# Performance work log

Measured on AMD Instinct MI355X. Metric: run time of the kernel, lower is better.

The kernel has to match this reference:

```python
import jax, jax.numpy as jnp
import numpy as np

NUM_OUT_POINTS = 8192  # init kwarg num_out_points


def setup_inputs() -> dict:
    key = jax.random.key(0)
    B, C, N = 32, 64, 65536
    x = jax.random.normal(key, (B, C, N), dtype=jnp.float32)
    return {"x": x}


def reference(x):
    # x: [B, C, N]. For each batch element draw a random permutation of the
    # N points and keep the first NUM_OUT_POINTS indices, then gather.
    B, C, N = x.shape
    keys = jax.random.split(jax.random.key(1), B)
    # idx: [B, K] int32, each row a prefix of an independent permutation of N
    idx = jax.vmap(lambda k: jax.random.permutation(k, N)[:NUM_OUT_POINTS])(keys)
    idx = idx.astype(jnp.int32)
    # gather along point axis: y[b, c, k] = x[b, c, idx[b, k]]
    y = jnp.take_along_axis(x, idx[:, None, :].astype(jnp.int64), axis=2)
    return y
```

## Files before the change

### kernel.cpp

```cpp
#include <hip/hip_runtime.h>
#include <stdint.h>

#define B_SZ 32
#define C_SZ 64
#define N_SZ 65536
#define K_SZ 8192
#define BCAP 384
#define NHEAD 48
#define JCAP 80

__device__ __forceinline__ uint32_t rotl32(uint32_t v, int r) {
  return (v << r) | (v >> (32 - r));
}

__device__ __forceinline__ void threefry2x32(uint32_t k0, uint32_t k1,
                                             uint32_t x0, uint32_t x1,
                                             uint32_t& o0, uint32_t& o1) {
  const uint32_t ks2 = k0 ^ k1 ^ 0x1BD11BDAu;
  x0 += k0; x1 += k1;
#define TF_R(r) { x0 += x1; x1 = rotl32(x1, (r)); x1 ^= x0; }
  TF_R(13) TF_R(15) TF_R(26) TF_R(6)   x0 += k1;  x1 += ks2 + 1u;
  TF_R(17) TF_R(29) TF_R(16) TF_R(24)  x0 += ks2; x1 += k0  + 2u;
  TF_R(13) TF_R(15) TF_R(26) TF_R(6)   x0 += k0;  x1 += k1  + 3u;
  TF_R(17) TF_R(29) TF_R(16) TF_R(24)  x0 += k1;  x1 += ks2 + 4u;
  TF_R(13) TF_R(15) TF_R(26) TF_R(6)   x0 += ks2; x1 += k0  + 5u;
#undef TF_R
  o0 = x0; o1 = x1;
}

__device__ __forceinline__ void subkey_for_round(int b, int round,
                                                 uint32_t& sk0, uint32_t& sk1) {
  uint32_t c0, c1;
  threefry2x32(0u, 1u, 0u, (uint32_t)b, c0, c1);
  for (int r = 0; r < round; ++r) {
    uint32_t n0, n1;
    threefry2x32(c0, c1, 0u, 0u, n0, n1);
    c0 = n0; c1 = n1;
  }
  threefry2x32(c0, c1, 0u, 1u, sk0, sk1);
}

__device__ __forceinline__ uint32_t block_excl_scan(uint32_t h, int t,
                                                    uint32_t* __restrict__ wsum) {
  const int lane = t & 63, w = t >> 6;
  uint32_t inc = h;
#pragma unroll
  for (int off = 1; off < 64; off <<= 1) {
    const uint32_t y = __shfl_up(inc, off, 64);
    if (lane >= off) inc += y;
  }
  if (lane == 63) wsum[w] = inc;
  __syncthreads();
  uint32_t woff = 0;
#pragma unroll
  for (int w2 = 0; w2 < 4; ++w2)
    if (w2 < w) woff += wsum[w2];
  return woff + inc - h;
}

__global__ __launch_bounds__(256) void zero_cnt(uint32_t* __restrict__ z) {
  z[blockIdx.x * 256 + threadIdx.x] = 0;
}

__global__ __launch_bounds__(256) void gen_scatter1(uint64_t* __restrict__ BVfix,
                                                    uint32_t* __restrict__ cnt1) {
  __shared__ uint32_t lcnt[256];
  __shared__ uint32_t gb[256];
  const int t = threadIdx.x, chunk = blockIdx.x, b = blockIdx.y;
  lcnt[t] = 0; __syncthreads();
  uint32_t sk0, sk1;
  subkey_for_round(b, 0, sk0, sk1);
  uint64_t v[16]; uint32_t r[16], dg[16];
  const int base = chunk * 4096;
#pragma unroll
  for (int e = 0; e < 16; ++e) {
    const int i = base + e * 256 + t;
    uint32_t o0, o1;
    threefry2x32(sk0, sk1, 0u, (uint32_t)i, o0, o1);
    const uint32_t bits = o0 ^ o1;
    v[e] = ((uint64_t)bits << 16) | (uint64_t)i;
    dg[e] = bits >> 24;
    r[e] = atomicAdd(&lcnt[dg[e]], 1u);
  }
  __syncthreads();
  if (lcnt[t]) gb[t] = atomicAdd(&cnt1[b * 256 + t], lcnt[t]);
  __syncthreads();
#pragma unroll
  for (int e = 0; e < 16; ++e) {
    const uint32_t slot = gb[dg[e]] + r[e];
    if (slot < BCAP)
      BVfix[((size_t)(b * 256 + dg[e])) * BCAP + slot] = v[e];
  }
}

__global__ __launch_bounds__(256) void rank_sort1(const uint64_t* __restrict__ BVfix,
                                                  const uint32_t* __restrict__ cnt1,
                                                  uint16_t* __restrict__ S1v) {
  __shared__ uint32_t sub[BCAP];
  __shared__ uint16_t dg[BCAP];
  __shared__ uint16_t idxt[BCAP];
  __shared__ uint32_t hist[256];
  __shared__ uint32_t cur[256];
  __shared__ uint32_t base2[257];
  __shared__ uint32_t wsum[4];
  __shared__ uint32_t sh_bn[2];
  const int t = threadIdx.x, u = blockIdx.x, b = blockIdx.y;

  {
    uint32_t hh = cnt1[b * 256 + t];
    if (hh > BCAP) hh = BCAP;
    const uint32_t excl0 = block_excl_scan(hh, t, wsum);
    if (t == u) { sh_bn[0] = excl0; sh_bn[1] = hh; }
  }
  __syncthreads();
  const uint32_t base = sh_bn[0];
  const uint32_t n = sh_bn[1];
  const uint64_t* __restrict__ g = BVfix + ((size_t)(b * 256 + u)) * BCAP;

  hist[t] = 0; __syncthreads();
  uint64_t rec[2] = {0, 0};
#pragma unroll
  for (int w = 0; w < 2; ++w) {
    const int e = t + w * 256;
    if (e < (int)n) {
      rec[w] = g[e];
      const uint32_t key = (uint32_t)(rec[w] >> 16);
      const uint32_t d = (key >> 16) & 0xFFu;
      sub[e] = ((key & 0xFFFFu) << 16) | (uint32_t)(rec[w] & 0xFFFFull);
      dg[e] = (uint16_t)d;
      atomicAdd(&hist[d], 1u);
    }
  }
  __syncthreads();
  const uint32_t h = hist[t];
  const uint32_t excl = block_excl_scan(h, t, wsum);
  base2[t] = excl;
  cur[t] = excl;
  if (t == 255) base2[256] = excl + h;
  __syncthreads();
#pragma unroll
  for (int w = 0; w < 2; ++w) {
    const int e = t + w * 256;
    if (e < (int)n) idxt[atomicAdd(&cur[dg[e]], 1u)] = (uint16_t)e;
  }
  __syncthreads();
  uint16_t* __restrict__ out = S1v + (size_t)b * N_SZ + base;
#pragma unroll
  for (int w = 0; w < 2; ++w) {
    const int e = t + w * 256;
    if (e < (int)n) {
      const uint32_t d = dg[e], s = sub[e];
      const uint32_t lo = base2[d], hi = base2[d + 1];
      uint32_t r = 0;
      for (uint32_t i = lo; i < hi; ++i) r += (sub[idxt[i]] < s) ? 1u : 0u;
      out[lo + r] = (uint16_t)(rec[w] & 0xFFFFull);
    }
  }
}

__global__ __launch_bounds__(256) void gen_scatter2(const uint16_t* __restrict__ S1v,
                                                    uint64_t* __restrict__ CVfix,
                                                    uint32_t* __restrict__ cnt2) {
  __shared__ uint32_t lcnt[256];
  __shared__ uint32_t gb[256];
  const int t = threadIdx.x, chunk = blockIdx.x, b = blockIdx.y;
  lcnt[t] = 0; __syncthreads();
  uint32_t sk0, sk1;
  subkey_for_round(b, 1, sk0, sk1);
  const uint16_t* __restrict__ s1 = S1v + (size_t)b * N_SZ;
  uint64_t v[16]; uint32_t r[16], dg[16];
  const int base = chunk * 4096;
#pragma unroll
  for (int e = 0; e < 16; ++e) {
    const int i = base + e * 256 + t;
    uint32_t o0, o1;
    threefry2x32(sk0, sk1, 0u, (uint32_t)i, o0, o1);
    const uint32_t bits = o0 ^ o1;
    dg[e] = bits >> 24;
    if (dg[e] < NHEAD) {
      v[e] = ((uint64_t)bits << 32) | ((uint64_t)(uint32_t)i << 16) | (uint64_t)s1[i];
      r[e] = atomicAdd(&lcnt[dg[e]], 1u);
    }
  }
  __syncthreads();
  if (t < NHEAD && lcnt[t]) gb[t] = atomicAdd(&cnt2[b * 256 + t], lcnt[t]);
  __syncthreads();
#pragma unroll
  for (int e = 0; e < 16; ++e) {
    if (dg[e] < NHEAD) {
      const uint32_t slot = gb[dg[e]] + r[e];
      if (slot < BCAP)
        CVfix[((size_t)(b * NHEAD + dg[e])) * BCAP + slot] = v[e];
    }
  }
}

__global__ __launch_bounds__(256) void finalize_rank(const uint64_t* __restrict__ CVfix,
                                                     const uint32_t* __restrict__ cnt2,
                                                     uint32_t* __restrict__ jcnt,
                                                     uint32_t* __restrict__ jb) {
  __shared__ uint32_t sub[BCAP];
  __shared__ uint16_t dg[BCAP];
  __shared__ uint16_t idxt[BCAP];
  __shared__ uint32_t hist[256];
  __shared__ uint32_t cur[256];
  __shared__ uint32_t base2[257];
  __shared__ uint32_t wsum[4];
  __shared__ uint32_t sh_bn[2];
  const int t = threadIdx.x, u = blockIdx.x, b = blockIdx.y;

  {
    uint32_t hh = 0;
    if (t < NHEAD) { hh = cnt2[b * 256 + t]; if (hh > BCAP) hh = BCAP; }
    const uint32_t excl0 = block_excl_scan(hh, t, wsum);
    if (t == u) { sh_bn[0] = excl0; sh_bn[1] = hh; }
  }
  __syncthreads();
  const uint32_t base = sh_bn[0];
  if (base >= K_SZ) return;
  const uint32_t n = sh_bn[1];
  const uint64_t* __restrict__ g = CVfix + ((size_t)(b * NHEAD + u)) * BCAP;

  hist[t] = 0; __syncthreads();
  uint64_t rec[2] = {0, 0};
#pragma unroll
  for (int w = 0; w < 2; ++w) {
    const int e = t + w * 256;
    if (e < (int)n) {
      rec[w] = g[e];
      const uint32_t key = (uint32_t)(rec[w] >> 32);
      const uint32_t d = (key >> 16) & 0xFFu;
      sub[e] = ((key & 0xFFFFu) << 16) | (uint32_t)((rec[w] >> 16) & 0xFFFFull);
      dg[e] = (uint16_t)d;
      atomicAdd(&hist[d], 1u);
    }
  }
  __syncthreads();
  const uint32_t h = hist[t];
  const uint32_t excl = block_excl_scan(h, t, wsum);
  base2[t] = excl;
  cur[t] = excl;
  if (t == 255) base2[256] = excl + h;
  __syncthreads();
#pragma unroll
  for (int w = 0; w < 2; ++w) {
    const int e = t + w * 256;
    if (e < (int)n) idxt[atomicAdd(&cur[dg[e]], 1u)] = (uint16_t)e;
  }
  __syncthreads();
#pragma unroll
  for (int w = 0; w < 2; ++w) {
    const int e = t + w * 256;
    if (e < (int)n) {
      const uint32_t d = dg[e], s = sub[e];
      const uint32_t lo = base2[d], hi = base2[d + 1];
      uint32_t r = 0;
      for (uint32_t i = lo; i < hi; ++i) r += (sub[idxt[i]] < s) ? 1u : 0u;
      const uint32_t q = base + lo + r;
      if (q < K_SZ) {
        const uint32_t j = (uint32_t)(rec[w] & 0xFFFFull);
        const uint32_t slot = atomicAdd(&jcnt[b * 256 + (j >> 8)], 1u);
        if (slot < JCAP)
          jb[((size_t)b * 256 + (j >> 8)) * JCAP + slot] = (j << 16) | q;
      }
    }
  }
}

__global__ __launch_bounds__(256) void compact_pairs(const uint32_t* __restrict__ jcnt,
                                                     const uint32_t* __restrict__ jb,
                                                     uint32_t* __restrict__ sp) {
  __shared__ uint32_t bases[256];
  __shared__ uint8_t map8[K_SZ];
  __shared__ uint32_t wsum[4];
  const int b = blockIdx.x, t = threadIdx.x;
  uint32_t c = jcnt[b * 256 + t];
  if (c > JCAP) c = JCAP;
  const uint32_t excl = block_excl_scan(c, t, wsum);
  bases[t] = excl;
  for (uint32_t i = 0; i < c; ++i)
    if (excl + i < K_SZ) map8[excl + i] = (uint8_t)t;
  __syncthreads();
  const uint32_t* __restrict__ jbb = jb + (size_t)b * 256 * JCAP;
  uint32_t* __restrict__ dst = sp + (size_t)b * K_SZ;
#pragma unroll 8
  for (int k = t; k < K_SZ; k += 256) {
    const uint32_t d = map8[k];
    dst[k] = jbb[d * JCAP + (k - bases[d])];
  }
}

__global__ __launch_bounds__(256) void gather_staged(const float* __restrict__ x,
                                                     const uint32_t* __restrict__ sp,
                                                     float* __restrict__ y) {
  __shared__ float row[K_SZ];
  const int t = threadIdx.x, c = blockIdx.x, b = blockIdx.y;
  const uint32_t* __restrict__ spb = sp + (size_t)b * K_SZ;
  const float* __restrict__ xr = x + ((size_t)b * C_SZ + c) * N_SZ;
#pragma unroll 8
  for (int w = 0; w < 32; ++w) {
    const uint32_t p = spb[w * 256 + t];
    row[p & 0xFFFFu] = xr[p >> 16];
  }
  __syncthreads();
  float4* __restrict__ yr4 = (float4*)(y + ((size_t)b * C_SZ + c) * K_SZ);
  const float4* __restrict__ r4 = (const float4*)row;
#pragma unroll
  for (int w = 0; w < 8; ++w) yr4[w * 256 + t] = r4[w * 256 + t];
}

extern "C" void kernel_launch(void* const* d_in, const int* in_sizes, int n_in,
                              void* d_out, int out_size, void* d_ws, size_t ws_size,
                              hipStream_t stream) {
  (void)in_sizes; (void)n_in; (void)out_size; (void)ws_size;
  const float* x = (const float*)d_in[0];
  float* y = (float*)d_out;

  char* base = (char*)d_out;
  uint64_t* BVfix = (uint64_t*)base;
  uint64_t* CVfix = (uint64_t*)(base + (26u << 20));
  uint16_t* S1v   = (uint16_t*)(base + (31u << 20));
  uint32_t* cnt1 = (uint32_t*)d_ws;
  uint32_t* cnt2 = (uint32_t*)((char*)d_ws + (32u << 10));
  uint32_t* jcnt = (uint32_t*)((char*)d_ws + (64u << 10));
  uint32_t* jb   = (uint32_t*)((char*)d_ws + (128u << 10));
  uint32_t* sp   = (uint32_t*)((char*)d_ws + (4u << 20));

  const dim3 blk(256);
  const dim3 ggen(16, B_SZ);

  zero_cnt<<<dim3(96), blk, 0, stream>>>(cnt1);
  gen_scatter1<<<ggen, blk, 0, stream>>>(BVfix, cnt1);
  rank_sort1<<<dim3(256, B_SZ), blk, 0, stream>>>(BVfix, cnt1, S1v);
  gen_scatter2<<<ggen, blk, 0, stream>>>(S1v, CVfix, cnt2);
  finalize_rank<<<dim3(NHEAD, B_SZ), blk, 0, stream>>>(CVfix, cnt2, jcnt, jb);
  compact_pairs<<<dim3(B_SZ), blk, 0, stream>>>(jcnt, jb, sp);
  gather_staged<<<dim3(C_SZ, B_SZ), blk, 0, stream>>>(x, sp, y);
}
```

Baseline: 187.0 us.

## Replace random-index gather with segment-streamed coalesced row reads and LDS scatter

The gather kernel now streams each full input row in eight coalesced float4 segments instead of issuing scattered 4-byte reads at sampled indices. compact_pairs records per-segment offsets into the bucket-sorted pair list. For each segment, the gather kernel builds a shared-memory map from source index to output slot and scatters only the selected values into the staged output row. Since nearly every cache line is already touched by the random sampling, this aims to turn uncoalesced traffic into full-bandwidth streaming. The cost is extra barriers, LDS map clears and more shared memory per block.

```diff
diff --git a/kernel.cpp b/kernel.cpp
--- a/kernel.cpp
+++ b/kernel.cpp
@@ -8,6 +8,7 @@
 #define BCAP 384
 #define NHEAD 48
 #define JCAP 80
+#define NSEG 8
 
 __device__ __forceinline__ uint32_t rotl32(uint32_t v, int r) {
   return (v << r) | (v >> (32 - r));
@@ -269,7 +270,8 @@
 
 __global__ __launch_bounds__(256) void compact_pairs(const uint32_t* __restrict__ jcnt,
                                                      const uint32_t* __restrict__ jb,
-                                                     uint32_t* __restrict__ sp) {
+                                                     uint32_t* __restrict__ sp,
+                                                     uint32_t* __restrict__ segoff) {
   __shared__ uint32_t bases[256];
   __shared__ uint8_t map8[K_SZ];
   __shared__ uint32_t wsum[4];
@@ -278,6 +280,8 @@
   if (c > JCAP) c = JCAP;
   const uint32_t excl = block_excl_scan(c, t, wsum);
   bases[t] = excl;
+  if ((t & 31) == 0) segoff[b * (NSEG + 1) + (t >> 5)] = excl;
+  if (t == 0) segoff[b * (NSEG + 1) + NSEG] = K_SZ;
   for (uint32_t i = 0; i < c; ++i)
     if (excl + i < K_SZ) map8[excl + i] = (uint8_t)t;
   __syncthreads();
@@ -290,19 +294,45 @@
   }
 }
 
-__global__ __launch_bounds__(256) void gather_staged(const float* __restrict__ x,
-                                                     const uint32_t* __restrict__ sp,
-                                                     float* __restrict__ y) {
+__global__ __launch_bounds__(256) void gather_streamed(const float* __restrict__ x,
+                                                       const uint32_t* __restrict__ sp,
+                                                       const uint32_t* __restrict__ segoff,
+                                                       float* __restrict__ y) {
+  __shared__ uint16_t jmap[8192];
   __shared__ float row[K_SZ];
   const int t = threadIdx.x, c = blockIdx.x, b = blockIdx.y;
   const uint32_t* __restrict__ spb = sp + (size_t)b * K_SZ;
+  const uint32_t* __restrict__ so = segoff + b * (NSEG + 1);
   const float* __restrict__ xr = x + ((size_t)b * C_SZ + c) * N_SZ;
-#pragma unroll 8
-  for (int w = 0; w < 32; ++w) {
-    const uint32_t p = spb[w * 256 + t];
-    row[p & 0xFFFFu] = xr[p >> 16];
-  }
-  __syncthreads();
+
+  for (int seg = 0; seg < NSEG; ++seg) {
+    uint32_t* jm32 = (uint32_t*)jmap;
+#pragma unroll
+    for (int w = 0; w < 16; ++w) jm32[w * 256 + t] = 0xFFFFFFFFu;
+    __syncthreads();
+    const uint32_t lo = so[seg], hi = so[seg + 1];
+    const uint32_t segj0 = (uint32_t)seg << 13;
+    for (uint32_t p = lo + t; p < hi; p += 256) {
+      const uint32_t e = spb[p];
+      jmap[(e >> 16) - segj0] = (uint16_t)(e & 0xFFFFu);
+    }
+    __syncthreads();
+    const float4* __restrict__ xs = (const float4*)(xr + ((size_t)seg << 13));
+#pragma unroll
+    for (int w = 0; w < 8; ++w) {
+      const float4 f = xs[w * 256 + t];
+      const uint32_t jb4 = (w * 256 + t) * 4;
+      const uint32_t q0 = jmap[jb4 + 0];
+      const uint32_t q1 = jmap[jb4 + 1];
+      const uint32_t q2 = jmap[jb4 + 2];
+      const uint32_t q3 = jmap[jb4 + 3];
+      if (q0 != 0xFFFFu) row[q0] = f.x;
+      if (q1 != 0xFFFFu) row[q1] = f.y;
+      if (q2 != 0xFFFFu) row[q2] = f.z;
+      if (q3 != 0xFFFFu) row[q3] = f.w;
+    }
+    __syncthreads();
+  }
   float4* __restrict__ yr4 = (float4*)(y + ((size_t)b * C_SZ + c) * K_SZ);
   const float4* __restrict__ r4 = (const float4*)row;
 #pragma unroll
@@ -324,6 +354,7 @@
   uint32_t* cnt2 = (uint32_t*)((char*)d_ws + (32u << 10));
   uint32_t* jcnt = (uint32_t*)((char*)d_ws + (64u << 10));
   uint32_t* jb   = (uint32_t*)((char*)d_ws + (128u << 10));
+  uint32_t* segoff = (uint32_t*)((char*)d_ws + (3u << 20));
   uint32_t* sp   = (uint32_t*)((char*)d_ws + (4u << 20));
 
   const dim3 blk(256);
@@ -334,6 +365,6 @@
   rank_sort1<<<dim3(256, B_SZ), blk, 0, stream>>>(BVfix, cnt1, S1v);
   gen_scatter2<<<ggen, blk, 0, stream>>>(S1v, CVfix, cnt2);
   finalize_rank<<<dim3(NHEAD, B_SZ), blk, 0, stream>>>(CVfix, cnt2, jcnt, jb);
-  compact_pairs<<<dim3(B_SZ), blk, 0, stream>>>(jcnt, jb, sp);
-  gather_staged<<<dim3(C_SZ, B_SZ), blk, 0, stream>>>(x, sp, y);
-}
+  compact_pairs<<<dim3(B_SZ), blk, 0, stream>>>(jcnt, jb, sp, segoff);
+  gather_streamed<<<dim3(C_SZ, B_SZ), blk, 0, stream>>>(x, sp, segoff, y);
+}
```

After: 266.1 us. 1.42x slower.
